# Optimization experiments

Measured on AMD Instinct MI355X. Metric: run time of the kernel, lower is better.

Reference implementation:

```python
import jax, jax.numpy as jnp
import numpy as np

ALPHA = 0.2  # LeakyReLU negative slope

def setup_inputs() -> dict:
    key = jax.random.key(0)
    k1, k2, k3, k4 = jax.random.split(key, 4)
    N, F_in, F_out = 8192, 512, 64
    x = jax.random.normal(k1, (N, F_in), dtype=jnp.float32)
    adj = jax.random.randint(k2, (N, N), 0, 2, dtype=jnp.int32)
    # xavier-normal-ish init
    weight = jax.random.normal(k3, (F_in, F_out), dtype=jnp.float32) * np.sqrt(2.0 / (F_in + F_out))
    a = jax.random.normal(k4, (2 * F_out, 1), dtype=jnp.float32) * np.sqrt(2.0 / (2 * F_out + 1))
    return {"x": x, "adj": adj, "weight": weight, "a": a}

def reference(x, adj, weight, a):
    # Wh: [N, F_out]
    Wh = x @ weight
    F_out = weight.shape[1]
    a1 = a[:F_out, 0]   # applies to source (row) node
    a2 = a[F_out:, 0]   # applies to target (col) node
    # e[i,j] = LeakyReLU(Wh[i]@a1 + Wh[j]@a2)  -- broadcast-add instead of O(N^2*2F) concat
    s1 = Wh @ a1        # [N]
    s2 = Wh @ a2        # [N]
    e = s1[:, None] + s2[None, :]              # [N, N]
    e = jnp.where(e > 0, e, ALPHA * e)         # LeakyReLU
    e = jnp.where(adj > 0, e, jnp.float32(-9e15))
    attention = jax.nn.softmax(e, axis=1)      # [N, N]
    h_prime = attention @ Wh                   # [N, F_out]
    return jax.nn.elu(h_prime)                 # concat=True -> ELU
```

## Files before the change

### kernel.cpp

```cpp
#include <hip/hip_runtime.h>
#include <hip/hip_bf16.h>
#include <cstdint>
#include <cstddef>

#define N_NODES 8192
#define F_IN 512
#define F_OUT 64
#define GAT_ALPHA 0.2f

typedef __attribute__((ext_vector_type(8))) short short8v;
typedef __attribute__((ext_vector_type(4))) float f32x4;

static __device__ __forceinline__ unsigned short f2bf(float f) {
    union { float f; unsigned u; } v; v.f = f;
    unsigned u = v.u + 0x7FFFu + ((v.u >> 16) & 1u);
    return (unsigned short)(u >> 16);
}
static __device__ __forceinline__ float bf2f(unsigned short b) {
    union { unsigned u; float f; } v; v.u = ((unsigned)b) << 16;
    return v.f;
}

__global__ __launch_bounds__(256)
void gat_wconv(const float* __restrict__ W, unsigned short* __restrict__ whf,
               unsigned short* __restrict__ wlf) {
    const int t = blockIdx.x * 256 + threadIdx.x;
    const int tile = t >> 6, lane = t & 63;
    const int kt = tile >> 2, ct = tile & 3;
    const int k0 = kt * 32 + ((lane >> 4) << 3);
    const int c  = ct * 16 + (lane & 15);
    short8v h, l;
    #pragma unroll
    for (int i = 0; i < 8; ++i) {
        float v = W[(size_t)(k0 + i) * F_OUT + c];
        unsigned short hb = f2bf(v);
        h[i] = (short)hb;
        l[i] = (short)f2bf(v - bf2f(hb));
    }
    const size_t dst = (size_t)tile * 512 + (size_t)lane * 8;
    *(short8v*)(whf + dst) = h;
    *(short8v*)(wlf + dst) = l;
}

__global__ __launch_bounds__(128)
void gat_prep(const float* __restrict__ x, const unsigned short* __restrict__ whf,
              const unsigned short* __restrict__ wlf, const float* __restrict__ a,
              unsigned short* __restrict__ whtf,
              float* __restrict__ s1, float* __restrict__ s2) {
    __shared__ unsigned short ldsT[64][40];
    const int tid = threadIdx.x;
    const int lane = tid & 63;
    const int wv = tid >> 6;
    const int l15 = lane & 15, g = lane >> 4;
    const int jt = blockIdx.x;
    const int row0 = jt * 32 + wv * 16;

    f32x4 acc[4] = {{0.f,0.f,0.f,0.f},{0.f,0.f,0.f,0.f},{0.f,0.f,0.f,0.f},{0.f,0.f,0.f,0.f}};

    const float* xp = x + (size_t)(row0 + l15) * F_IN + g * 8;
    for (int kt = 0; kt < 16; ++kt) {
        float4 v0 = *(const float4*)(xp);
        float4 v1 = *(const float4*)(xp + 4);
        xp += 32;
        float vv[8] = {v0.x, v0.y, v0.z, v0.w, v1.x, v1.y, v1.z, v1.w};
        short8v xh, xl;
        #pragma unroll
        for (int i = 0; i < 8; ++i) {
            unsigned short hb = f2bf(vv[i]);
            xh[i] = (short)hb;
            xl[i] = (short)f2bf(vv[i] - bf2f(hb));
        }
        const unsigned short* wp = whf + (size_t)(kt * 4) * 512 + (size_t)lane * 8;
        const unsigned short* lp = wlf + (size_t)(kt * 4) * 512 + (size_t)lane * 8;
        #pragma unroll
        for (int ct = 0; ct < 4; ++ct) {
            short8v wh = *(const short8v*)(wp + ct * 512);
            short8v wl = *(const short8v*)(lp + ct * 512);
            acc[ct] = __builtin_amdgcn_mfma_f32_16x16x32_bf16(xh, wh, acc[ct], 0, 0, 0);
            acc[ct] = __builtin_amdgcn_mfma_f32_16x16x32_bf16(xl, wh, acc[ct], 0, 0, 0);
            acc[ct] = __builtin_amdgcn_mfma_f32_16x16x32_bf16(xh, wl, acc[ct], 0, 0, 0);
        }
    }

    #pragma unroll
    for (int r = 0; r < 4; ++r) {
        float p1 = 0.f, p2 = 0.f;
        #pragma unroll
        for (int ct = 0; ct < 4; ++ct) {
            p1 = fmaf(acc[ct][r], a[ct * 16 + l15], p1);
            p2 = fmaf(acc[ct][r], a[64 + ct * 16 + l15], p2);
        }
        p1 += __shfl_xor(p1, 1); p2 += __shfl_xor(p2, 1);
        p1 += __shfl_xor(p1, 2); p2 += __shfl_xor(p2, 2);
        p1 += __shfl_xor(p1, 4); p2 += __shfl_xor(p2, 4);
        p1 += __shfl_xor(p1, 8); p2 += __shfl_xor(p2, 8);
        if (l15 == 0) {
            s1[row0 + g * 4 + r] = p1;
            s2[row0 + g * 4 + r] = p2;
        }
    }

    #pragma unroll
    for (int ct = 0; ct < 4; ++ct) {
        ushort4 pk;
        pk.x = f2bf(acc[ct][0]); pk.y = f2bf(acc[ct][1]);
        pk.z = f2bf(acc[ct][2]); pk.w = f2bf(acc[ct][3]);
        *(ushort4*)&ldsT[ct * 16 + l15][wv * 16 + g * 4] = pk;
    }
    __syncthreads();

    #pragma unroll
    for (int fl = 0; fl < 2; ++fl) {
        const int ft = wv * 2 + fl;
        short8v sv = *(const short8v*)&ldsT[ft * 16 + l15][g * 8];
        *(short8v*)(whtf + ((size_t)jt * 4 + ft) * 512 + (size_t)lane * 8) = sv;
    }
}

__global__ __launch_bounds__(512)
void gat_main(const int* __restrict__ adj, const unsigned short* __restrict__ whtf,
              const float* __restrict__ s1, const float* __restrict__ s2,
              float* __restrict__ out) {
    __shared__ float nums[8][16][64];
    __shared__ float dens[8][16];
    const int tid  = threadIdx.x;
    const int lane = tid & 63;
    const int wv   = tid >> 6;
    const int l15  = lane & 15, g = lane >> 4;
    const int r0   = blockIdx.x * 16;
    const int row  = r0 + l15;
    const float s1r = s1[row];
    const int j0 = wv * 1024;

    const int*   ap  = adj + (size_t)row * N_NODES + j0 + g * 8;
    const float* s2p = s2 + j0 + g * 8;
    const unsigned short* bp = whtf + ((size_t)(j0 >> 5) * 4) * 512 + (size_t)lane * 8;

    f32x4 acc0 = {0.f, 0.f, 0.f, 0.f};
    f32x4 acc1 = acc0, acc2 = acc0, acc3 = acc0;
    float dsum = 0.f;

    for (int t = 0; t < 32; ++t) {
        int4   aj0 = *(const int4*)ap;
        int4   aj1 = *(const int4*)(ap + 4);
        float4 sa  = *(const float4*)s2p;
        float4 sb  = *(const float4*)(s2p + 4);
        short8v afrag;
        float e, w;
        unsigned short hb;
        #define GAT_EL(idx, ajv, s2v) do { \
            e = s1r + (s2v); e = e > 0.f ? e : GAT_ALPHA * e; \
            w = (ajv) > 0 ? __expf(e) : 0.f; \
            hb = f2bf(w); dsum += bf2f(hb); afrag[idx] = (short)hb; } while (0);
        GAT_EL(0, aj0.x, sa.x) GAT_EL(1, aj0.y, sa.y)
        GAT_EL(2, aj0.z, sa.z) GAT_EL(3, aj0.w, sa.w)
        GAT_EL(4, aj1.x, sb.x) GAT_EL(5, aj1.y, sb.y)
        GAT_EL(6, aj1.z, sb.z) GAT_EL(7, aj1.w, sb.w)
        #undef GAT_EL

        short8v b0 = *(const short8v*)(bp);
        short8v b1 = *(const short8v*)(bp + 512);
        short8v b2 = *(const short8v*)(bp + 1024);
        short8v b3 = *(const short8v*)(bp + 1536);
        acc0 = __builtin_amdgcn_mfma_f32_16x16x32_bf16(afrag, b0, acc0, 0, 0, 0);
        acc1 = __builtin_amdgcn_mfma_f32_16x16x32_bf16(afrag, b1, acc1, 0, 0, 0);
        acc2 = __builtin_amdgcn_mfma_f32_16x16x32_bf16(afrag, b2, acc2, 0, 0, 0);
        acc3 = __builtin_amdgcn_mfma_f32_16x16x32_bf16(afrag, b3, acc3, 0, 0, 0);

        ap += 32; s2p += 32; bp += 2048;
    }

    dsum += __shfl_xor(dsum, 16);
    dsum += __shfl_xor(dsum, 32);

    #pragma unroll
    for (int r = 0; r < 4; ++r) {
        nums[wv][g * 4 + r][0 * 16 + l15] = acc0[r];
        nums[wv][g * 4 + r][1 * 16 + l15] = acc1[r];
        nums[wv][g * 4 + r][2 * 16 + l15] = acc2[r];
        nums[wv][g * 4 + r][3 * 16 + l15] = acc3[r];
    }
    if (lane < 16) dens[wv][lane] = dsum;
    __syncthreads();

    for (int o = tid; o < 16 * 64; o += 512) {
        const int r = o >> 6, f = o & 63;
        float num = 0.f, den = 0.f;
        #pragma unroll
        for (int q = 0; q < 8; ++q) { num += nums[q][r][f]; den += dens[q][r]; }
        float h = num / den;
        out[(size_t)(r0 + r) * 64 + f] = h > 0.f ? h : __expf(h) - 1.f;
    }
}

extern "C" void kernel_launch(void* const* d_in, const int* in_sizes, int n_in,
                              void* d_out, int out_size, void* d_ws, size_t ws_size,
                              hipStream_t stream) {
    const float* x      = (const float*)d_in[0];
    const int*   adj    = (const int*)d_in[1];
    const float* weight = (const float*)d_in[2];
    const float* a      = (const float*)d_in[3];
    float* out = (float*)d_out;

    char* ws = (char*)d_ws;
    unsigned short* whtf = (unsigned short*)ws;
    float* s1            = (float*)(ws + 1048576);
    float* s2            = (float*)(ws + 1048576 + 32768);
    unsigned short* whf  = (unsigned short*)(ws + 1048576 + 65536);
    unsigned short* wlf  = (unsigned short*)(ws + 1048576 + 65536 + 65536);

    gat_wconv<<<16, 256, 0, stream>>>(weight, whf, wlf);
    gat_prep<<<N_NODES / 32, 128, 0, stream>>>(x, whf, wlf, a, whtf, s1, s2);
    gat_main<<<N_NODES / 16, 512, 0, stream>>>(adj, whtf, s1, s2, out);
}
```

Measured before the change: 105.1 us.

## Prefetch adjacency tiles, use exp2 with prescaled scores and packed bf16 converts

The main loop now loads the next iteration's adjacency and s2 values before computing the current one, which is a software prefetch. The adjacency stream uses nontemporal loads. The scores are pre-multiplied by log2(e) so the kernel can call the hardware exp2 directly. The LeakyReLU becomes an fmax, and the manual bf16 rounding is replaced by v_cvt_pk_bf16_f32. The denominator now sums the unrounded fp32 weights instead of the bf16-rounded ones, which slightly changes the numerics, and the prefetch raises register pressure.

```diff
diff --git a/kernel.cpp b/kernel.cpp
--- a/kernel.cpp
+++ b/kernel.cpp
@@ -6,10 +6,12 @@
 #define N_NODES 8192
 #define F_IN 512
 #define F_OUT 64
-#define GAT_ALPHA 0.2f
+#define LOG2E 1.44269504f
 
 typedef __attribute__((ext_vector_type(8))) short short8v;
 typedef __attribute__((ext_vector_type(4))) float f32x4;
+typedef __attribute__((ext_vector_type(4))) int i32x4;
+typedef __attribute__((ext_vector_type(4))) unsigned int u32x4;
 
 static __device__ __forceinline__ unsigned short f2bf(float f) {
     union { float f; unsigned u; } v; v.f = f;
@@ -19,6 +21,11 @@
 static __device__ __forceinline__ float bf2f(unsigned short b) {
     union { unsigned u; float f; } v; v.u = ((unsigned)b) << 16;
     return v.f;
+}
+static __device__ __forceinline__ unsigned cvt_pk_bf16(float lo, float hi) {
+    unsigned r;
+    asm("v_cvt_pk_bf16_f32 %0, %1, %2" : "=v"(r) : "v"(lo), "v"(hi));
+    return r;
 }
 
 __global__ __launch_bounds__(256)
@@ -95,8 +102,8 @@
         p1 += __shfl_xor(p1, 4); p2 += __shfl_xor(p2, 4);
         p1 += __shfl_xor(p1, 8); p2 += __shfl_xor(p2, 8);
         if (l15 == 0) {
-            s1[row0 + g * 4 + r] = p1;
-            s2[row0 + g * 4 + r] = p2;
+            s1[row0 + g * 4 + r] = p1 * LOG2E;
+            s2[row0 + g * 4 + r] = p2 * LOG2E;
         }
     }
 
@@ -132,42 +139,58 @@
     const float s1r = s1[row];
     const int j0 = wv * 1024;
 
-    const int*   ap  = adj + (size_t)row * N_NODES + j0 + g * 8;
-    const float* s2p = s2 + j0 + g * 8;
+    const i32x4*  ap  = (const i32x4*)(adj + (size_t)row * N_NODES + j0 + g * 8);
+    const float4* s2p = (const float4*)(s2 + j0 + g * 8);
     const unsigned short* bp = whtf + ((size_t)(j0 >> 5) * 4) * 512 + (size_t)lane * 8;
 
     f32x4 acc0 = {0.f, 0.f, 0.f, 0.f};
     f32x4 acc1 = acc0, acc2 = acc0, acc3 = acc0;
     float dsum = 0.f;
 
+    i32x4  aj0 = __builtin_nontemporal_load(ap);
+    i32x4  aj1 = __builtin_nontemporal_load(ap + 1);
+    float4 sa  = s2p[0];
+    float4 sb  = s2p[1];
+
     for (int t = 0; t < 32; ++t) {
-        int4   aj0 = *(const int4*)ap;
-        int4   aj1 = *(const int4*)(ap + 4);
-        float4 sa  = *(const float4*)s2p;
-        float4 sb  = *(const float4*)(s2p + 4);
-        short8v afrag;
-        float e, w;
-        unsigned short hb;
-        #define GAT_EL(idx, ajv, s2v) do { \
-            e = s1r + (s2v); e = e > 0.f ? e : GAT_ALPHA * e; \
-            w = (ajv) > 0 ? __expf(e) : 0.f; \
-            hb = f2bf(w); dsum += bf2f(hb); afrag[idx] = (short)hb; } while (0);
-        GAT_EL(0, aj0.x, sa.x) GAT_EL(1, aj0.y, sa.y)
-        GAT_EL(2, aj0.z, sa.z) GAT_EL(3, aj0.w, sa.w)
-        GAT_EL(4, aj1.x, sb.x) GAT_EL(5, aj1.y, sb.y)
-        GAT_EL(6, aj1.z, sb.z) GAT_EL(7, aj1.w, sb.w)
-        #undef GAT_EL
+        const i32x4  caj0 = aj0, caj1 = aj1;
+        const float4 csa = sa, csb = sb;
+        if (t < 31) {
+            ap  += 8; s2p += 8;
+            aj0 = __builtin_nontemporal_load(ap);
+            aj1 = __builtin_nontemporal_load(ap + 1);
+            sa  = s2p[0];
+            sb  = s2p[1];
+        }
 
         short8v b0 = *(const short8v*)(bp);
         short8v b1 = *(const short8v*)(bp + 512);
         short8v b2 = *(const short8v*)(bp + 1024);
         short8v b3 = *(const short8v*)(bp + 1536);
+        bp += 2048;
+
+        float w0, w1, w2, w3, w4, w5, w6, w7;
+        #define GAT_EL(wvar, ajv, s2v) do { \
+            float e = s1r + (s2v); e = fmaxf(e, 0.2f * e); \
+            float ex = __builtin_amdgcn_exp2f(e); \
+            wvar = ((ajv) > 0) ? ex : 0.f; dsum += wvar; } while (0);
+        GAT_EL(w0, caj0[0], csa.x) GAT_EL(w1, caj0[1], csa.y)
+        GAT_EL(w2, caj0[2], csa.z) GAT_EL(w3, caj0[3], csa.w)
+        GAT_EL(w4, caj1[0], csb.x) GAT_EL(w5, caj1[1], csb.y)
+        GAT_EL(w6, caj1[2], csb.z) GAT_EL(w7, caj1[3], csb.w)
+        #undef GAT_EL
+
+        u32x4 au;
+        au[0] = cvt_pk_bf16(w0, w1);
+        au[1] = cvt_pk_bf16(w2, w3);
+        au[2] = cvt_pk_bf16(w4, w5);
+        au[3] = cvt_pk_bf16(w6, w7);
+        short8v afrag = __builtin_bit_cast(short8v, au);
+
         acc0 = __builtin_amdgcn_mfma_f32_16x16x32_bf16(afrag, b0, acc0, 0, 0, 0);
         acc1 = __builtin_amdgcn_mfma_f32_16x16x32_bf16(afrag, b1, acc1, 0, 0, 0);
         acc2 = __builtin_amdgcn_mfma_f32_16x16x32_bf16(afrag, b2, acc2, 0, 0, 0);
         acc3 = __builtin_amdgcn_mfma_f32_16x16x32_bf16(afrag, b3, acc3, 0, 0, 0);
-
-        ap += 32; s2p += 32; bp += 2048;
     }
 
     dsum += __shfl_xor(dsum, 16);
```

Measured after the change: 127.7 us. 21.5% more time.
